# Kernel tuning notes

Measured on AMD Instinct MI355X. Metric: run time of the kernel, lower is better.

Reference implementation:

```python
import jax, jax.numpy as jnp
import numpy as np

N_NODES = 50000
N_EDGES = 800000
D_IN = 64
D_OUT = 64


def setup_inputs() -> dict:
    key = jax.random.key(0)
    k = jax.random.split(key, 5)
    stdv = 1.0 / np.sqrt(D_OUT)
    X = jax.random.normal(k[0], (N_NODES, D_IN), jnp.float32)
    weights = jax.random.uniform(k[1], (D_IN, D_OUT), jnp.float32, -stdv, stdv)
    attention_w = jax.random.normal(k[2], (1, 1), jnp.float32)
    # edge list: row = destination (segment) ids, sorted (CSR-like); col = source ids
    row = jnp.sort(jax.random.randint(k[3], (N_EDGES,), 0, N_NODES, jnp.int32))
    col = jax.random.randint(k[4], (N_EDGES,), 0, N_NODES, jnp.int32)
    return {"X": X, "weights": weights, "attention_w": attention_w, "row": row, "col": col}


def reference(X, weights, attention_w, row, col):
    # dense linear
    Xp = X @ weights  # [N, D_OUT]
    # SDDMM: per-edge dot product between dst and src transformed features
    edge_feature = jnp.einsum('ed,ed->e', Xp[row], Xp[col])  # [E]
    # scale by scalar attention weight (n_heads = 1)
    edge_attn = edge_feature * attention_w[0, 0]  # [E]
    # SpMM aggregation: out[i] = sum_{e: row[e]=i} edge_attn[e] * Xp[col[e]]
    out = jax.ops.segment_sum(edge_attn[:, None] * Xp[col], row,
                              num_segments=X.shape[0])  # [N, D_OUT]
    return out
```

## Files before the change

### kernel.cpp

```cpp
#include <hip/hip_runtime.h>
#include <hip/hip_fp16.h>

#define D 64

typedef _Float16 h16;
typedef h16 h16x2 __attribute__((ext_vector_type(2)));

__device__ __forceinline__ h16x2 u2h(unsigned int u) {
    union { unsigned int i; h16x2 h; } t; t.i = u; return t.h;
}

__device__ __forceinline__ float dot8_f16(uint4 a, uint4 b, float c) {
#if __has_builtin(__builtin_amdgcn_fdot2)
    c = __builtin_amdgcn_fdot2(u2h(a.x), u2h(b.x), c, false);
    c = __builtin_amdgcn_fdot2(u2h(a.y), u2h(b.y), c, false);
    c = __builtin_amdgcn_fdot2(u2h(a.z), u2h(b.z), c, false);
    c = __builtin_amdgcn_fdot2(u2h(a.w), u2h(b.w), c, false);
    return c;
#else
    float2 t, s;
    t = __half22float2(*(const __half2*)&a.x); s = __half22float2(*(const __half2*)&b.x);
    c = fmaf(t.x, s.x, c); c = fmaf(t.y, s.y, c);
    t = __half22float2(*(const __half2*)&a.y); s = __half22float2(*(const __half2*)&b.y);
    c = fmaf(t.x, s.x, c); c = fmaf(t.y, s.y, c);
    t = __half22float2(*(const __half2*)&a.z); s = __half22float2(*(const __half2*)&b.z);
    c = fmaf(t.x, s.x, c); c = fmaf(t.y, s.y, c);
    t = __half22float2(*(const __half2*)&a.w); s = __half22float2(*(const __half2*)&b.w);
    c = fmaf(t.x, s.x, c); c = fmaf(t.y, s.y, c);
    return c;
#endif
}

__global__ __launch_bounds__(256) void prep_kernel(const float* __restrict__ X,
                                                   const float* __restrict__ W,
                                                   const int* __restrict__ row,
                                                   __half* __restrict__ Xp,
                                                   int* __restrict__ rowptr,
                                                   int nNodes, int nEdges,
                                                   int gemmBlocks) {
    if ((int)blockIdx.x >= gemmBlocks) {
        int e = (blockIdx.x - gemmBlocks) * 256 + threadIdx.x;
        if (e >= nEdges) return;
        int r = row[e];
        int rprev = (e == 0) ? -1 : row[e - 1];
        for (int q = rprev + 1; q <= r; ++q) rowptr[q] = e;
        if (e == nEdges - 1) {
            for (int q = r + 1; q <= nNodes; ++q) rowptr[q] = nEdges;
        }
        return;
    }
    int lane = threadIdx.x & 63;
    int wave = (blockIdx.x * 256 + threadIdx.x) >> 6;
    int nWaves = gemmBlocks * 4;

    float w[D];
#pragma unroll
    for (int k = 0; k < D; ++k) w[k] = W[k * D + lane];

    for (int r = wave; r < nNodes; r += nWaves) {
        int rr = __builtin_amdgcn_readfirstlane(r);
        const float4* xr = (const float4*)(X + (size_t)rr * D);
        float acc = 0.f;
#pragma unroll
        for (int k4 = 0; k4 < D / 4; ++k4) {
            float4 xv = xr[k4];
            acc = fmaf(xv.x, w[4 * k4 + 0], acc);
            acc = fmaf(xv.y, w[4 * k4 + 1], acc);
            acc = fmaf(xv.z, w[4 * k4 + 2], acc);
            acc = fmaf(xv.w, w[4 * k4 + 3], acc);
        }
        Xp[(size_t)rr * D + lane] = __float2half(acc);
    }
}

__global__ __launch_bounds__(256) void fused_kernel(const __half* __restrict__ Xp,
                                                    const int* __restrict__ rowptr,
                                                    const int* __restrict__ col,
                                                    const float* __restrict__ attn_w,
                                                    float* __restrict__ out,
                                                    int nNodes) {
    int lane = threadIdx.x & 63;
    int waveId = (blockIdx.x * 256 + threadIdx.x) >> 6;
    int g = lane >> 3;
    int j = lane & 7;

    int node = waveId * 8 + g;
    bool active = node < nNodes;
    int nd = active ? node : 0;

    int eStart = rowptr[nd];
    int eEnd   = active ? rowptr[nd + 1] : eStart;

    const uint4* XpV = (const uint4*)Xp;
    uint4 xr = XpV[(size_t)nd * 8 + j];

    __half2 acc[4];
#pragma unroll
    for (int q = 0; q < 4; ++q) acc[q] = __float2half2_rn(0.f);

    bool v[8]; uint4 raw[8];
#pragma unroll
    for (int u = 0; u < 8; ++u) {
        int ee = eStart + u;
        v[u] = ee < eEnd;
        int cc = col[v[u] ? ee : 0];
        raw[u] = XpV[(size_t)cc * 8 + j];
    }

    for (int e = eStart; e < eEnd; e += 8) {
        bool v2[8]; uint4 raw2[8];
#pragma unroll
        for (int u = 0; u < 8; ++u) {
            int ee = e + 8 + u;
            v2[u] = ee < eEnd;
            int cc = col[v2[u] ? ee : 0];
            raw2[u] = XpV[(size_t)cc * 8 + j];
        }
        float p[8];
#pragma unroll
        for (int u = 0; u < 8; ++u) p[u] = dot8_f16(xr, raw[u], 0.f);
#pragma unroll
        for (int off = 1; off < 8; off <<= 1)
#pragma unroll
            for (int u = 0; u < 8; ++u) p[u] += __shfl_xor(p[u], off, 64);
#pragma unroll
        for (int u = 0; u < 8; ++u) {
            __half2 sh = __float2half2_rn(v[u] ? p[u] : 0.f);
            const __half2* xh = (const __half2*)&raw[u];
#pragma unroll
            for (int q = 0; q < 4; ++q) acc[q] = __hfma2(sh, xh[q], acc[q]);
        }
#pragma unroll
        for (int u = 0; u < 8; ++u) { v[u] = v2[u]; raw[u] = raw2[u]; }
    }

    if (active) {
        float attn = attn_w[0];
        float2 f0 = __half22float2(acc[0]);
        float2 f1 = __half22float2(acc[1]);
        float2 f2 = __half22float2(acc[2]);
        float2 f3 = __half22float2(acc[3]);
        float4* o = (float4*)(out + (size_t)node * D + 8 * j);
        o[0] = make_float4(attn * f0.x, attn * f0.y, attn * f1.x, attn * f1.y);
        o[1] = make_float4(attn * f2.x, attn * f2.y, attn * f3.x, attn * f3.y);
    }
}

extern "C" void kernel_launch(void* const* d_in, const int* in_sizes, int n_in,
                              void* d_out, int out_size, void* d_ws, size_t ws_size,
                              hipStream_t stream) {
    const float* X    = (const float*)d_in[0];
    const float* W    = (const float*)d_in[1];
    const float* attn = (const float*)d_in[2];
    const int*   row  = (const int*)d_in[3];
    const int*   col  = (const int*)d_in[4];
    float* out = (float*)d_out;

    int nNodes = in_sizes[0] / D;
    int nEdges = in_sizes[3];

    __half* Xp  = (__half*)d_ws;
    int* rowptr = (int*)((char*)d_ws + (size_t)nNodes * D * sizeof(__half));

    int gemmBlocks = 1024;
    int rpBlocks   = (nEdges + 255) / 256;
    prep_kernel<<<gemmBlocks + rpBlocks, 256, 0, stream>>>(X, W, row, Xp, rowptr,
                                                           nNodes, nEdges, gemmBlocks);

    int waves = (nNodes + 7) / 8;
    fused_kernel<<<(waves + 3) / 4, 256, 0, stream>>>(Xp, rowptr, col, attn, out, nNodes);
}
```

Measured before the change: 105.3 us.

## Quantize gathered source features to per-row int8 with offset correction

The prep kernel now also writes a per-row symmetric int8 copy of the transformed features (stored as uint8 with +128 bias) plus one float scale per node. The fused gather kernel reads 8 bytes per lane instead of 16 for each neighbour, which halves the random-gather traffic. It corrects for the bias algebraically using precomputed row sums and a running scale sum. In exchange there is extra unpack/convert ALU work, a scale load per edge, and int8 quantization error that may exceed the tolerance.

```diff
diff --git a/kernel.cpp b/kernel.cpp
--- a/kernel.cpp
+++ b/kernel.cpp
@@ -3,38 +3,41 @@
 
 #define D 64
 
-typedef _Float16 h16;
-typedef h16 h16x2 __attribute__((ext_vector_type(2)));
-
-__device__ __forceinline__ h16x2 u2h(unsigned int u) {
-    union { unsigned int i; h16x2 h; } t; t.i = u; return t.h;
-}
-
-__device__ __forceinline__ float dot8_f16(uint4 a, uint4 b, float c) {
-#if __has_builtin(__builtin_amdgcn_fdot2)
-    c = __builtin_amdgcn_fdot2(u2h(a.x), u2h(b.x), c, false);
-    c = __builtin_amdgcn_fdot2(u2h(a.y), u2h(b.y), c, false);
-    c = __builtin_amdgcn_fdot2(u2h(a.z), u2h(b.z), c, false);
-    c = __builtin_amdgcn_fdot2(u2h(a.w), u2h(b.w), c, false);
-    return c;
-#else
-    float2 t, s;
-    t = __half22float2(*(const __half2*)&a.x); s = __half22float2(*(const __half2*)&b.x);
-    c = fmaf(t.x, s.x, c); c = fmaf(t.y, s.y, c);
-    t = __half22float2(*(const __half2*)&a.y); s = __half22float2(*(const __half2*)&b.y);
-    c = fmaf(t.x, s.x, c); c = fmaf(t.y, s.y, c);
-    t = __half22float2(*(const __half2*)&a.z); s = __half22float2(*(const __half2*)&b.z);
-    c = fmaf(t.x, s.x, c); c = fmaf(t.y, s.y, c);
-    t = __half22float2(*(const __half2*)&a.w); s = __half22float2(*(const __half2*)&b.w);
-    c = fmaf(t.x, s.x, c); c = fmaf(t.y, s.y, c);
-    return c;
+__device__ __forceinline__ float ub0(unsigned u) {
+#if __has_builtin(__builtin_amdgcn_cvt_f32_ubyte0)
+    return __builtin_amdgcn_cvt_f32_ubyte0(u);
+#else
+    return (float)(u & 0xFF);
+#endif
+}
+__device__ __forceinline__ float ub1(unsigned u) {
+#if __has_builtin(__builtin_amdgcn_cvt_f32_ubyte1)
+    return __builtin_amdgcn_cvt_f32_ubyte1(u);
+#else
+    return (float)((u >> 8) & 0xFF);
+#endif
+}
+__device__ __forceinline__ float ub2(unsigned u) {
+#if __has_builtin(__builtin_amdgcn_cvt_f32_ubyte2)
+    return __builtin_amdgcn_cvt_f32_ubyte2(u);
+#else
+    return (float)((u >> 16) & 0xFF);
+#endif
+}
+__device__ __forceinline__ float ub3(unsigned u) {
+#if __has_builtin(__builtin_amdgcn_cvt_f32_ubyte3)
+    return __builtin_amdgcn_cvt_f32_ubyte3(u);
+#else
+    return (float)(u >> 24);
 #endif
 }
 
 __global__ __launch_bounds__(256) void prep_kernel(const float* __restrict__ X,
                                                    const float* __restrict__ W,
                                                    const int* __restrict__ row,
-                                                   __half* __restrict__ Xp,
+                                                   __half* __restrict__ Xp16,
+                                                   unsigned char* __restrict__ Q,
+                                                   float* __restrict__ scales,
                                                    int* __restrict__ rowptr,
                                                    int nNodes, int nEdges,
                                                    int gemmBlocks) {
@@ -69,11 +72,25 @@
             acc = fmaf(xv.z, w[4 * k4 + 2], acc);
             acc = fmaf(xv.w, w[4 * k4 + 3], acc);
         }
-        Xp[(size_t)rr * D + lane] = __float2half(acc);
-    }
-}
-
-__global__ __launch_bounds__(256) void fused_kernel(const __half* __restrict__ Xp,
+        Xp16[(size_t)rr * D + lane] = __float2half(acc);
+
+        float m = fabsf(acc);
+#pragma unroll
+        for (int off = 1; off < 64; off <<= 1)
+            m = fmaxf(m, __shfl_xor(m, off, 64));
+
+        float inv   = (m > 0.f) ? 127.f / m : 0.f;
+        float scale = (m > 0.f) ? m / 127.f : 0.f;
+        int q = (int)rintf(acc * inv);
+        q = q < -127 ? -127 : (q > 127 ? 127 : q);
+        Q[(size_t)rr * D + lane] = (unsigned char)(q + 128);
+        if (lane == 0) scales[rr] = scale;
+    }
+}
+
+__global__ __launch_bounds__(256) void fused_kernel(const __half* __restrict__ Xp16,
+                                                    const unsigned char* __restrict__ Q,
+                                                    const float* __restrict__ scales,
                                                     const int* __restrict__ rowptr,
                                                     const int* __restrict__ col,
                                                     const float* __restrict__ attn_w,
@@ -91,58 +108,86 @@
     int eStart = rowptr[nd];
     int eEnd   = active ? rowptr[nd + 1] : eStart;
 
-    const uint4* XpV = (const uint4*)Xp;
-    uint4 xr = XpV[(size_t)nd * 8 + j];
-
-    __half2 acc[4];
-#pragma unroll
-    for (int q = 0; q < 4; ++q) acc[q] = __float2half2_rn(0.f);
-
-    bool v[8]; uint4 raw[8];
+    const uint4* Xp16V = (const uint4*)Xp16;
+    uint4 xru = Xp16V[(size_t)nd * 8 + j];
+    float xrf[8];
+    {
+        float2 t;
+        t = __half22float2(*(const __half2*)&xru.x); xrf[0] = t.x; xrf[1] = t.y;
+        t = __half22float2(*(const __half2*)&xru.y); xrf[2] = t.x; xrf[3] = t.y;
+        t = __half22float2(*(const __half2*)&xru.z); xrf[4] = t.x; xrf[5] = t.y;
+        t = __half22float2(*(const __half2*)&xru.w); xrf[6] = t.x; xrf[7] = t.y;
+    }
+    float sx = 0.f;
+#pragma unroll
+    for (int q = 0; q < 8; ++q) sx += xrf[q];
+#pragma unroll
+    for (int off = 1; off < 8; off <<= 1) sx += __shfl_xor(sx, off, 64);
+    float SX128 = 128.f * sx;
+
+    const uint2* QV = (const uint2*)Q;
+
+    float acc[8] = {0.f, 0.f, 0.f, 0.f, 0.f, 0.f, 0.f, 0.f};
+    float SS = 0.f;
+
+    bool v[8]; uint2 raw[8]; float sc[8];
 #pragma unroll
     for (int u = 0; u < 8; ++u) {
         int ee = eStart + u;
         v[u] = ee < eEnd;
         int cc = col[v[u] ? ee : 0];
-        raw[u] = XpV[(size_t)cc * 8 + j];
+        raw[u] = QV[(size_t)cc * 8 + j];
+        sc[u]  = scales[cc];
     }
 
     for (int e = eStart; e < eEnd; e += 8) {
-        bool v2[8]; uint4 raw2[8];
+        bool v2[8]; uint2 raw2[8]; float sc2[8];
 #pragma unroll
         for (int u = 0; u < 8; ++u) {
             int ee = e + 8 + u;
             v2[u] = ee < eEnd;
             int cc = col[v2[u] ? ee : 0];
-            raw2[u] = XpV[(size_t)cc * 8 + j];
-        }
-        float p[8];
-#pragma unroll
-        for (int u = 0; u < 8; ++u) p[u] = dot8_f16(xr, raw[u], 0.f);
+            raw2[u] = QV[(size_t)cc * 8 + j];
+            sc2[u]  = scales[cc];
+        }
+        float d[8];
+#pragma unroll
+        for (int u = 0; u < 8; ++u) {
+            unsigned a = raw[u].x, b = raw[u].y;
+            float s = 0.f;
+            s = fmaf(xrf[0], ub0(a), s); s = fmaf(xrf[1], ub1(a), s);
+            s = fmaf(xrf[2], ub2(a), s); s = fmaf(xrf[3], ub3(a), s);
+            s = fmaf(xrf[4], ub0(b), s); s = fmaf(xrf[5], ub1(b), s);
+            s = fmaf(xrf[6], ub2(b), s); s = fmaf(xrf[7], ub3(b), s);
+            d[u] = s;
+        }
 #pragma unroll
         for (int off = 1; off < 8; off <<= 1)
 #pragma unroll
-            for (int u = 0; u < 8; ++u) p[u] += __shfl_xor(p[u], off, 64);
+            for (int u = 0; u < 8; ++u) d[u] += __shfl_xor(d[u], off, 64);
 #pragma unroll
         for (int u = 0; u < 8; ++u) {
-            __half2 sh = __float2half2_rn(v[u] ? p[u] : 0.f);
-            const __half2* xh = (const __half2*)&raw[u];
-#pragma unroll
-            for (int q = 0; q < 4; ++q) acc[q] = __hfma2(sh, xh[q], acc[q]);
-        }
-#pragma unroll
-        for (int u = 0; u < 8; ++u) { v[u] = v2[u]; raw[u] = raw2[u]; }
+            float p  = sc[u] * (d[u] - SX128);
+            float ss = v[u] ? p * sc[u] : 0.f;
+            SS += ss;
+            unsigned a = raw[u].x, b = raw[u].y;
+            acc[0] = fmaf(ss, ub0(a), acc[0]); acc[1] = fmaf(ss, ub1(a), acc[1]);
+            acc[2] = fmaf(ss, ub2(a), acc[2]); acc[3] = fmaf(ss, ub3(a), acc[3]);
+            acc[4] = fmaf(ss, ub0(b), acc[4]); acc[5] = fmaf(ss, ub1(b), acc[5]);
+            acc[6] = fmaf(ss, ub2(b), acc[6]); acc[7] = fmaf(ss, ub3(b), acc[7]);
+        }
+#pragma unroll
+        for (int u = 0; u < 8; ++u) { v[u] = v2[u]; raw[u] = raw2[u]; sc[u] = sc2[u]; }
     }
 
     if (active) {
         float attn = attn_w[0];
-        float2 f0 = __half22float2(acc[0]);
-        float2 f1 = __half22float2(acc[1]);
-        float2 f2 = __half22float2(acc[2]);
-        float2 f3 = __half22float2(acc[3]);
+        float corr = 128.f * SS;
         float4* o = (float4*)(out + (size_t)node * D + 8 * j);
-        o[0] = make_float4(attn * f0.x, attn * f0.y, attn * f1.x, attn * f1.y);
-        o[1] = make_float4(attn * f2.x, attn * f2.y, attn * f3.x, attn * f3.y);
+        o[0] = make_float4(attn * (acc[0] - corr), attn * (acc[1] - corr),
+                           attn * (acc[2] - corr), attn * (acc[3] - corr));
+        o[1] = make_float4(attn * (acc[4] - corr), attn * (acc[5] - corr),
+                           attn * (acc[6] - corr), attn * (acc[7] - corr));
     }
 }
 
@@ -159,14 +204,18 @@
     int nNodes = in_sizes[0] / D;
     int nEdges = in_sizes[3];
 
-    __half* Xp  = (__half*)d_ws;
-    int* rowptr = (int*)((char*)d_ws + (size_t)nNodes * D * sizeof(__half));
+    unsigned char* Q = (unsigned char*)d_ws;
+    float* scales = (float*)(Q + (size_t)nNodes * D);
+    __half* Xp16  = (__half*)(scales + nNodes);
+    int* rowptr   = (int*)((char*)Xp16 + (size_t)nNodes * D * sizeof(__half));
 
     int gemmBlocks = 1024;
     int rpBlocks   = (nEdges + 255) / 256;
-    prep_kernel<<<gemmBlocks + rpBlocks, 256, 0, stream>>>(X, W, row, Xp, rowptr,
-                                                           nNodes, nEdges, gemmBlocks);
+    prep_kernel<<<gemmBlocks + rpBlocks, 256, 0, stream>>>(X, W, row, Xp16, Q, scales,
+                                                           rowptr, nNodes, nEdges,
+                                                           gemmBlocks);
 
     int waves = (nNodes + 7) / 8;
-    fused_kernel<<<(waves + 3) / 4, 256, 0, stream>>>(Xp, rowptr, col, attn, out, nNodes);
-}
+    fused_kernel<<<(waves + 3) / 4, 256, 0, stream>>>(Xp16, Q, scales, rowptr, col,
+                                                      attn, out, nNodes);
+}
```

After: 114.4 us. +8.6%, slower.
